# Optimization experiments

Hardware: AMD Instinct MI355X
Metric: run time of the kernel (lower is better)

## Reference

```python
import jax, jax.numpy as jnp
import numpy as np
from jax import lax

BATCH = 2
COUNT = 5
OUT = 125


def _bins(n, out=OUT):
    # PyTorch adaptive_max_pool2d bin boundaries: start=floor(i*n/out), end=ceil((i+1)*n/out)
    i = np.arange(out)
    s = (i * n) // out
    e = -((-(i + 1) * n) // out)
    m = int((e - s).max())
    idx = s[:, None] + np.arange(m)[None, :]
    return np.minimum(idx, n - 1), idx < e[:, None]


def _apool(img):
    # adaptive max pool 2d of [H,W] -> [OUT,OUT]; H,W are concrete Python ints
    H, W = img.shape
    ri, rv = _bins(H)
    ci, cv = _bins(W)
    r = jnp.where(rv[:, :, None], img[ri], -jnp.inf).max(axis=1)       # [OUT, W]
    return jnp.where(cv[None], r[:, ci], -jnp.inf).max(axis=2)         # [OUT, OUT]


def _conv(x, w, b):
    y = lax.conv_general_dilated(x, w, (1, 1), 'VALID', dimension_numbers=('NCHW', 'OIHW', 'NCHW'))
    return y + b[None, :, None, None]


def _bn(x, g, be, m, v):
    inv = g * lax.rsqrt(v + 1e-5)
    return x * inv[None, :, None, None] + (be - m * inv)[None, :, None, None]


def _pool(x, k, s):
    return lax.reduce_window(x, -np.inf, lax.max, (1, 1, k, k), (1, 1, s, s), 'VALID')


def _forward(x, ROI, roi_layer, w1, b1, g1, be1, m1, v1, w2, b2, g2, be2, m2, v2,
             w3, b3, g3, be3, m3, v3, w4, b4, g4, be4, m4, v4, fw1, fb1, fw2, fb2, fw3, fb3):
    ROI = np.asarray(ROI)
    rl = int(roi_layer)
    roiX = jax.nn.relu(_bn(_conv(x, w1, b1), g1, be1, m1, v1))  # [2,3,252,252]
    crops = []
    for k in range(BATCH):
        xs = []
        for j in range(rl):
            for i in range(COUNT):
                y1, y2, x1, x2 = (int(v) for v in ROI[k, i, 0])
                y1 = int(y1 * 0.9); y2 = int(y2 * 0.9); x2 = int(x2 * 0.9); x1 = int(x1 * 0.9)
                xs.append(_apool(roiX[k, j, y1:y2, x1:x2]))
        crops.append(xs)
    # original code prepends each batch's crop list -> batch order reversed; .numpy() detaches grads
    xb = lax.stop_gradient(jnp.stack(crops[1] + crops[0]).reshape(BATCH, COUNT * rl, OUT, OUT))
    norX = _pool(jax.nn.relu(_bn(_conv(x, w2, b2), g2, be2, m2, v2)), 4, 2)  # [2,20,125,125]
    h = jnp.concatenate([norX, xb], axis=1)                                   # [2,35,125,125]
    h = _pool(jax.nn.relu(_bn(_conv(h, w3, b3), g3, be3, m3, v3)), 2, 2)      # [2,50,60,60]
    h = _pool(jax.nn.relu(_bn(_conv(h, w4, b4), g4, be4, m4, v4)), 2, 2)      # [2,25,28,28]
    h = h.reshape(BATCH, -1)                                                  # [2,19600]
    h = jax.nn.relu(h @ fw1 + fb1)
    h = jax.nn.relu(h @ fw2 + fb2)
    h = jax.nn.relu(h @ fw3 + fb3)
    return jax.nn.softmax(h, axis=1)


def setup_inputs() -> dict:
    key = jax.random.key(0)
    ks = jax.random.split(key, 8)
    rng = np.random.default_rng(0)
    y1 = rng.integers(0, 100, (BATCH, COUNT))
    y2 = np.minimum(y1 + rng.integers(60, 150, (BATCH, COUNT)), 251)
    x1 = rng.integers(0, 100, (BATCH, COUNT))
    x2 = np.minimum(x1 + rng.integers(60, 150, (BATCH, COUNT)), 251)
    ROI = jnp.asarray(np.stack([y1, y2, x1, x2], -1)[:, :, None, :].astype(np.int32))
    d = {'x': jax.random.normal(ks[0], (BATCH, 1, 256, 256), jnp.float32), 'ROI': ROI, 'roi_layer': 3}
    d.update(w1=jax.random.normal(ks[1], (3, 1, 5, 5)) * 0.05, b1=jnp.zeros(3), g1=jnp.ones(3), be1=jnp.zeros(3), m1=jnp.zeros(3), v1=jnp.ones(3))
    d.update(w2=jax.random.normal(ks[2], (20, 1, 5, 5)) * 0.05, b2=jnp.zeros(20), g2=jnp.ones(20), be2=jnp.zeros(20), m2=jnp.zeros(20), v2=jnp.ones(20))
    d.update(w3=jax.random.normal(ks[3], (50, 35, 5, 5)) * 0.05, b3=jnp.zeros(50), g3=jnp.ones(50), be3=jnp.zeros(50), m3=jnp.zeros(50), v3=jnp.ones(50))
    d.update(w4=jax.random.normal(ks[4], (25, 50, 5, 5)) * 0.05, b4=jnp.zeros(25), g4=jnp.ones(25), be4=jnp.zeros(25), m4=jnp.zeros(25), v4=jnp.ones(25))
    d.update(fw1=jax.random.normal(ks[5], (25 * 28 * 28, 1024)) * 0.01, fb1=jnp.zeros(1024),
             fw2=jax.random.normal(ks[6], (1024, 32)) * 0.05, fb2=jnp.zeros(32),
             fw3=jax.random.normal(ks[7], (32, 2)) * 0.05, fb3=jnp.zeros(2))
    return d


def reference(x, ROI, roi_layer, w1, b1, g1, be1, m1, v1, w2, b2, g2, be2, m2, v2,
              w3, b3, g3, be3, m3, v3, w4, b4, g4, be4, m4, v4, fw1, fb1, fw2, fb2, fw3, fb3):
    return _forward(x, ROI, roi_layer, w1, b1, g1, be1, m1, v1, w2, b2, g2, be2, m2, v2,
                    w3, b3, g3, be3, m3, v3, w4, b4, g4, be4, m4, v4, fw1, fb1, fw2, fb2, fw3, fb3)
```

## Files before the change

### kernel.cpp

```cpp
#include <hip/hip_runtime.h>
#include <math.h>


#define RL 3
#define NCH 35

__global__ __launch_bounds__(256) void conv2_roi(
    const float* __restrict__ x, const int* __restrict__ ROI,
    const float* __restrict__ w2, const float* __restrict__ b2, const float* __restrict__ g2,
    const float* __restrict__ be2, const float* __restrict__ m2, const float* __restrict__ v2,
    const float* __restrict__ w1, const float* __restrict__ b1, const float* __restrict__ g1,
    const float* __restrict__ be1, const float* __restrict__ m1, const float* __restrict__ v1,
    float* __restrict__ h1) {
    int i = blockIdx.x * 256 + threadIdx.x;
    if (i >= 125 * 125) return;
    int oy = i / 125, ox = i % 125;
    if (blockIdx.y < 40) {
        int c = blockIdx.y % 20;
        int bi = blockIdx.y / 20;
        const float* xp = x + bi * 256 * 256 + (2 * oy) * 256 + 2 * ox;
        float wl[25];
#pragma unroll
        for (int k = 0; k < 25; k++) wl[k] = w2[c * 25 + k];
        float in[8][8];
#pragma unroll
        for (int r = 0; r < 8; r++)
#pragma unroll
            for (int k = 0; k < 4; k++) {
                float2 v2v = *(const float2*)(xp + r * 256 + 2 * k);
                in[r][2 * k] = v2v.x;
                in[r][2 * k + 1] = v2v.y;
            }
        float inv = g2[c] * rsqrtf(v2[c] + 1e-5f);
        float sh = (b2[c] - m2[c]) * inv + be2[c];
        float mx = -INFINITY;
#pragma unroll
        for (int py = 0; py < 4; py++) {
#pragma unroll
            for (int px = 0; px < 4; px++) {
                float acc = 0.f;
#pragma unroll
                for (int ky = 0; ky < 5; ky++)
#pragma unroll
                    for (int kx = 0; kx < 5; kx++)
                        acc = fmaf(in[py + ky][px + kx], wl[ky * 5 + kx], acc);
                mx = fmaxf(mx, fmaxf(acc * inv + sh, 0.f));
            }
        }
        h1[((bi * NCH + c) * 125 + oy) * 125 + ox] = mx;
    } else {
        int yz = blockIdx.y - 40;
        int bi = yz / 15;
        int cc = yz % 15;
        int sb = 1 - bi;
        int j = cc / 5;
        int ri = cc % 5;
        const int* rp = ROI + (sb * 5 + ri) * 4;
        int y1 = (9 * rp[0]) / 10;
        int y2 = (9 * rp[1]) / 10;
        int x1 = (9 * rp[2]) / 10;
        int x2 = (9 * rp[3]) / 10;
        int H = y2 - y1;
        int W = x2 - x1;
        int sy = (oy * H) / 125, ey = ((oy + 1) * H + 124) / 125;
        int sx = (ox * W) / 125, ex = ((ox + 1) * W + 124) / 125;
        float wl[25];
#pragma unroll
        for (int k = 0; k < 25; k++) wl[k] = w1[j * 25 + k];
        float inv = g1[j] * rsqrtf(v1[j] + 1e-5f);
        float sh = (b1[j] - m1[j]) * inv + be1[j];
        const float* xp = x + sb * 256 * 256;
        float mx = -INFINITY;
        for (int r = sy; r < ey; r++) {
            for (int c2 = sx; c2 < ex; c2++) {
                int Y = y1 + r, X = x1 + c2;
                float acc = 0.f;
#pragma unroll
                for (int ky = 0; ky < 5; ky++)
#pragma unroll
                    for (int kx = 0; kx < 5; kx++)
                        acc = fmaf(xp[(Y + ky) * 256 + X + kx], wl[ky * 5 + kx], acc);
                mx = fmaxf(mx, fmaxf(acc * inv + sh, 0.f));
            }
        }
        h1[((bi * NCH + 20 + cc) * 125 + oy) * 125 + ox] = mx;
    }
}

template <int IW, int PO, int CI, int CO, int G, int NG>
__global__ __launch_bounds__(256) void conv_partial_q(
    const float* __restrict__ in, const float* __restrict__ w,
    float* __restrict__ pac) {
    __shared__ float tile[4][2][20][24];

    const int wid = threadIdx.x >> 6;
    const int lane = threadIdx.x & 63;
    const int sy = lane >> 3, sx = lane & 7;
    const int ng = blockIdx.z % NG;
    const int bi = blockIdx.z / NG;
    const int s = wid;
    const int co0 = ng * G;
    constexpr int CPS = (CI + 3) / 4;
    const int ci0 = s * CPS;
    const int ci1 = (ci0 + CPS < CI) ? ci0 + CPS : CI;
    const int px0 = (8 * (int)blockIdx.x < PO - 8) ? 8 * (int)blockIdx.x : PO - 8;
    const int py0 = (8 * (int)blockIdx.y < PO - 8) ? 8 * (int)blockIdx.y : PO - 8;
    const int px = px0 + sx, py = py0 + sy;
    const float* ip = in + (size_t)bi * CI * IW * IW + (size_t)(2 * py0) * IW + 2 * px0;

    int cw[G];
#pragma unroll
    for (int gg = 0; gg < G; gg++) cw[gg] = (co0 + gg < CO) ? co0 + gg : CO - 1;

    float2 sreg[4];
    auto loadstage = [&](int ci) {
        const float* src = ip + (size_t)ci * IW * IW;
#pragma unroll
        for (int k = 0; k < 4; k++) {
            int p = lane + k * 64;
            if (p < 200) {
                int r = p / 10, c2 = (p % 10) * 2;
                sreg[k] = *(const float2*)(src + r * IW + c2);
            }
        }
    };
    auto writestage = [&](int buf) {
#pragma unroll
        for (int k = 0; k < 4; k++) {
            int p = lane + k * 64;
            if (p < 200) {
                int r = p / 10, c2 = (p % 10) * 2;
                *(float2*)&tile[wid][buf][r][c2] = sreg[k];
            }
        }
    };

    loadstage(ci0);
    writestage(0);
    float acc[G][4];
#pragma unroll
    for (int gg = 0; gg < G; gg++)
#pragma unroll
        for (int q = 0; q < 4; q++) acc[gg][q] = 0.f;

    for (int ci = ci0; ci < ci1; ci++) {
        const int cur = (ci - ci0) & 1;
        if (ci + 1 < ci1) loadstage(ci + 1);
        float2 p[6][3];
#pragma unroll
        for (int r = 0; r < 6; r++)
#pragma unroll
            for (int c = 0; c < 3; c++)
                p[r][c] = *(const float2*)&tile[wid][cur][2 * sy + r][2 * sx + 2 * c];
#define E(r, cc) (((cc) & 1) ? p[r][(cc) >> 1].y : p[r][(cc) >> 1].x)
#pragma unroll
        for (int gg = 0; gg < G; gg++) {
            const float* wk = w + ((size_t)cw[gg] * CI + ci) * 25;
#pragma unroll
            for (int ky = 0; ky < 5; ky++) {
#pragma unroll
                for (int kx = 0; kx < 5; kx++) {
                    float wv = wk[ky * 5 + kx];
                    acc[gg][0] = fmaf(E(ky, kx), wv, acc[gg][0]);
                    acc[gg][1] = fmaf(E(ky, kx + 1), wv, acc[gg][1]);
                    acc[gg][2] = fmaf(E(ky + 1, kx), wv, acc[gg][2]);
                    acc[gg][3] = fmaf(E(ky + 1, kx + 1), wv, acc[gg][3]);
                }
            }
        }
#undef E
        if (ci + 1 < ci1) writestage(cur ^ 1);
    }

    constexpr int CW = 2 * PO;
#pragma unroll
    for (int gg = 0; gg < G; gg++) {
        int co = co0 + gg;
        if (co < CO) {
            size_t base = (((size_t)(s * 2 + bi) * CO + co) * CW + 2 * py) * CW + 2 * px;
            float2 r0 = {acc[gg][0], acc[gg][1]};
            float2 r1 = {acc[gg][2], acc[gg][3]};
            *(float2*)&pac[base] = r0;
            *(float2*)&pac[base + CW] = r1;
        }
    }
}

template <int PO, int CO, int INIT>
__global__ __launch_bounds__(256) void conv_finish(
    const float* __restrict__ pac,
    const float* __restrict__ b, const float* __restrict__ g,
    const float* __restrict__ be, const float* __restrict__ m,
    const float* __restrict__ v, float* __restrict__ out,
    const float* __restrict__ fb1, float* __restrict__ fc1o) {
    int idx = blockIdx.x * 256 + threadIdx.x;
    if (INIT && idx < 2048) fc1o[idx] = fb1[idx & 1023];
    int total = 2 * CO * PO * PO;
    if (idx >= total) return;
    int px = idx % PO;
    int t = idx / PO;
    int py = t % PO; t /= PO;
    int co = t % CO;
    int bi = t / CO;
    constexpr int CW = 2 * PO;
    constexpr size_t SS = (size_t)2 * CO * CW * CW;
    size_t base = (((size_t)bi * CO + co) * CW + 2 * py) * CW + 2 * px;
    float s00 = 0.f, s01 = 0.f, s10 = 0.f, s11 = 0.f;
#pragma unroll
    for (int s = 0; s < 4; s++) {
        float2 a0 = *(const float2*)&pac[base + s * SS];
        float2 a1 = *(const float2*)&pac[base + s * SS + CW];
        s00 += a0.x; s01 += a0.y; s10 += a1.x; s11 += a1.y;
    }
    float inv = g[co] * rsqrtf(v[co] + 1e-5f);
    float sh = (b[co] - m[co]) * inv + be[co];
    float q0 = fmaxf(s00 * inv + sh, 0.f);
    float q1 = fmaxf(s01 * inv + sh, 0.f);
    float q2 = fmaxf(s10 * inv + sh, 0.f);
    float q3 = fmaxf(s11 * inv + sh, 0.f);
    out[idx] = fmaxf(fmaxf(q0, q1), fmaxf(q2, q3));
}

#define CHUNK 50
__global__ void fc1_mm(const float* __restrict__ h, const float* __restrict__ w,
                       float* __restrict__ out) {
    __shared__ float sh[2][CHUNK];
    int o = blockIdx.x * 256 + threadIdx.x;
    int i0 = blockIdx.y * CHUNK;
    if (threadIdx.x < 2 * CHUNK) {
        int r = threadIdx.x / CHUNK, t = threadIdx.x % CHUNK;
        sh[r][t] = h[r * 19600 + i0 + t];
    }
    __syncthreads();
    float a0 = 0.f, a1 = 0.f;
    const float* wp = w + (size_t)i0 * 1024 + o;
#pragma unroll
    for (int i = 0; i < CHUNK; i++) {
        float wv = wp[(size_t)i * 1024];
        a0 = fmaf(sh[0][i], wv, a0);
        a1 = fmaf(sh[1][i], wv, a1);
    }
    atomicAdd(&out[o], a0);
    atomicAdd(&out[1024 + o], a1);
}

__global__ void head(const float* __restrict__ fc1o, const float* __restrict__ fw2,
                     const float* __restrict__ fb2, const float* __restrict__ fw3,
                     const float* __restrict__ fb3, float* __restrict__ out) {
    int bi = blockIdx.x;
    __shared__ float h[1024];
    __shared__ float red[256];
    __shared__ float s2[32];
    for (int i = threadIdx.x; i < 1024; i += 256) h[i] = fmaxf(fc1o[bi * 1024 + i], 0.f);
    __syncthreads();
    int o = threadIdx.x >> 3;
    int part = threadIdx.x & 7;
    float a = 0.f;
    for (int i = part * 128; i < part * 128 + 128; i++) a += h[i] * fw2[i * 32 + o];
    red[threadIdx.x] = a;
    __syncthreads();
    if (part == 0) {
        float s = 0.f;
        for (int p = 0; p < 8; p++) s += red[(o << 3) + p];
        s2[o] = fmaxf(s + fb2[o], 0.f);
    }
    __syncthreads();
    if (threadIdx.x == 0) {
        float z0 = fb3[0], z1 = fb3[1];
        for (int i = 0; i < 32; i++) {
            z0 += s2[i] * fw3[i * 2];
            z1 += s2[i] * fw3[i * 2 + 1];
        }
        z0 = fmaxf(z0, 0.f);
        z1 = fmaxf(z1, 0.f);
        float mx = fmaxf(z0, z1);
        float e0 = expf(z0 - mx), e1 = expf(z1 - mx);
        float s = e0 + e1;
        out[bi * 2 + 0] = e0 / s;
        out[bi * 2 + 1] = e1 / s;
    }
}

extern "C" void kernel_launch(void* const* d_in, const int* in_sizes, int n_in,
                              void* d_out, int out_size, void* d_ws, size_t ws_size,
                              hipStream_t stream) {
    const float* x   = (const float*)d_in[0];
    const int*   ROI = (const int*)d_in[1];
    const float* w1 = (const float*)d_in[3];
    const float* b1 = (const float*)d_in[4];
    const float* g1 = (const float*)d_in[5];
    const float* be1 = (const float*)d_in[6];
    const float* m1 = (const float*)d_in[7];
    const float* v1 = (const float*)d_in[8];
    const float* w2 = (const float*)d_in[9];
    const float* b2 = (const float*)d_in[10];
    const float* g2 = (const float*)d_in[11];
    const float* be2 = (const float*)d_in[12];
    const float* m2 = (const float*)d_in[13];
    const float* v2 = (const float*)d_in[14];
    const float* w3 = (const float*)d_in[15];
    const float* b3 = (const float*)d_in[16];
    const float* g3 = (const float*)d_in[17];
    const float* be3 = (const float*)d_in[18];
    const float* m3 = (const float*)d_in[19];
    const float* v3 = (const float*)d_in[20];
    const float* w4 = (const float*)d_in[21];
    const float* b4 = (const float*)d_in[22];
    const float* g4 = (const float*)d_in[23];
    const float* be4 = (const float*)d_in[24];
    const float* m4 = (const float*)d_in[25];
    const float* v4 = (const float*)d_in[26];
    const float* fw1 = (const float*)d_in[27];
    const float* fb1 = (const float*)d_in[28];
    const float* fw2 = (const float*)d_in[29];
    const float* fb2 = (const float*)d_in[30];
    const float* fw3 = (const float*)d_in[31];
    const float* fb3 = (const float*)d_in[32];
    float* out = (float*)d_out;

    float* ws = (float*)d_ws;
    float* h1   = ws;
    float* p3   = h1 + 1093750;
    float* p4   = p3 + 360000;
    float* fc1o = p4 + 39200;
    float* pac3 = fc1o + 2048;
    float* pac4 = pac3;

    {
        dim3 grd((125 * 125 + 255) / 256, 70);
        conv2_roi<<<grd, 256, 0, stream>>>(x, ROI, w2, b2, g2, be2, m2, v2,
                                           w1, b1, g1, be1, m1, v1, h1);
    }
    {
        dim3 grd(8, 8, 2 * 13);
        conv_partial_q<125, 60, NCH, 50, 4, 13><<<grd, 256, 0, stream>>>(h1, w3, pac3);
    }
    {
        int total = 2 * 50 * 60 * 60;
        conv_finish<60, 50, 0><<<(total + 255) / 256, 256, 0, stream>>>(
            pac3, b3, g3, be3, m3, v3, p3, nullptr, nullptr);
    }
    {
        dim3 grd(4, 4, 2 * 13);
        conv_partial_q<60, 28, 50, 25, 2, 13><<<grd, 256, 0, stream>>>(p3, w4, pac4);
    }
    {
        int total = 2 * 25 * 28 * 28;
        conv_finish<28, 25, 1><<<(total + 255) / 256, 256, 0, stream>>>(
            pac4, b4, g4, be4, m4, v4, p4, fb1, fc1o);
    }
    {
        dim3 grd(4, 392);
        fc1_mm<<<grd, 256, 0, stream>>>(p4, fw1, fc1o);
    }
    head<<<2, 256, 0, stream>>>(fc1o, fw2, fb2, fw3, fb3, out);
}
```

Before: 136.9 us.

## Pad conv weights to float4 rows and split partial conv into 64-thread blocks

Extra blocks in the first kernel copy the conv3 and conv4 weights into a buffer whose 5x5 filters are padded to 28 floats. The partial conv kernels can then fetch each filter with seven float4 loads, double-buffered across output-channel groups. Each partial conv kernel is also restructured from 256-thread blocks, where four waves split the input channels, into 64-thread single-wave blocks with the channel split moved into the grid. The output-channel group size also changes. The aim is fewer scalar weight loads, better latency hiding and more blocks in flight, at the cost of extra register pressure and a small weight-repack pass run on every call.

```diff
diff --git a/kernel.cpp b/kernel.cpp
--- a/kernel.cpp
+++ b/kernel.cpp
@@ -11,7 +11,20 @@
     const float* __restrict__ be2, const float* __restrict__ m2, const float* __restrict__ v2,
     const float* __restrict__ w1, const float* __restrict__ b1, const float* __restrict__ g1,
     const float* __restrict__ be1, const float* __restrict__ m1, const float* __restrict__ v1,
+    const float* __restrict__ w3, const float* __restrict__ w4,
+    float* __restrict__ wp3, float* __restrict__ wp4,
     float* __restrict__ h1) {
+    if (blockIdx.y >= 70) {
+        const float* src = (blockIdx.y == 70) ? w3 : w4;
+        float* dst = (blockIdx.y == 70) ? wp3 : wp4;
+        int rows = (blockIdx.y == 70) ? 50 * 35 : 25 * 50;
+        int total = rows * 28;
+        for (int i = blockIdx.x * 256 + threadIdx.x; i < total; i += gridDim.x * 256) {
+            int t = i % 28, r = i / 28;
+            dst[i] = (t < 25) ? src[r * 25 + t] : 0.f;
+        }
+        return;
+    }
     int i = blockIdx.x * 256 + threadIdx.x;
     if (i >= 125 * 125) return;
     int oy = i / 125, ox = i % 125;
@@ -87,20 +100,20 @@
     }
 }
 
-template <int IW, int PO, int CI, int CO, int G, int NG>
-__global__ __launch_bounds__(256) void conv_partial_q(
-    const float* __restrict__ in, const float* __restrict__ w,
+template <int IW, int PO, int CI, int CO, int G, int NG, int NS>
+__global__ __launch_bounds__(64, 4) void conv_partial(
+    const float* __restrict__ in, const float* __restrict__ wp,
     float* __restrict__ pac) {
-    __shared__ float tile[4][2][20][24];
-
-    const int wid = threadIdx.x >> 6;
-    const int lane = threadIdx.x & 63;
+    __shared__ float tile[2][20][24];
+
+    const int lane = threadIdx.x;
     const int sy = lane >> 3, sx = lane & 7;
-    const int ng = blockIdx.z % NG;
-    const int bi = blockIdx.z / NG;
-    const int s = wid;
+    int z = blockIdx.z;
+    const int ng = z % NG; z /= NG;
+    const int s = z % NS;
+    const int bi = z / NS;
     const int co0 = ng * G;
-    constexpr int CPS = (CI + 3) / 4;
+    constexpr int CPS = (CI + NS - 1) / NS;
     const int ci0 = s * CPS;
     const int ci1 = (ci0 + CPS < CI) ? ci0 + CPS : CI;
     const int px0 = (8 * (int)blockIdx.x < PO - 8) ? 8 * (int)blockIdx.x : PO - 8;
@@ -130,47 +143,64 @@
             int p = lane + k * 64;
             if (p < 200) {
                 int r = p / 10, c2 = (p % 10) * 2;
-                *(float2*)&tile[wid][buf][r][c2] = sreg[k];
+                *(float2*)&tile[buf][r][c2] = sreg[k];
             }
         }
     };
+
+    float4 wA[7], wB[7];
+    auto wload = [&](float4(&wr)[7], int gg, int ci) {
+        const float* src = wp + ((size_t)cw[gg] * CI + ci) * 28;
+#pragma unroll
+        for (int k = 0; k < 7; k++) wr[k] = *(const float4*)(src + 4 * k);
+    };
+
+    float acc[G][4];
+#pragma unroll
+    for (int gg = 0; gg < G; gg++)
+#pragma unroll
+        for (int q = 0; q < 4; q++) acc[gg][q] = 0.f;
+
+#define WE(W, t) ((t) % 4 == 0 ? W[(t) / 4].x : (t) % 4 == 1 ? W[(t) / 4].y : (t) % 4 == 2 ? W[(t) / 4].z : W[(t) / 4].w)
+#define FMAG(W, gg)                                                            \
+    {                                                                          \
+        _Pragma("unroll") for (int ky = 0; ky < 5; ky++) {                     \
+            _Pragma("unroll") for (int kx = 0; kx < 5; kx++) {                 \
+                float wv = WE(W, ky * 5 + kx);                                 \
+                float e00 = ((kx)&1) ? p[ky][kx >> 1].y : p[ky][kx >> 1].x;    \
+                float e01 = ((kx + 1) & 1) ? p[ky][(kx + 1) >> 1].y : p[ky][(kx + 1) >> 1].x; \
+                float e10 = ((kx)&1) ? p[ky + 1][kx >> 1].y : p[ky + 1][kx >> 1].x; \
+                float e11 = ((kx + 1) & 1) ? p[ky + 1][(kx + 1) >> 1].y : p[ky + 1][(kx + 1) >> 1].x; \
+                acc[gg][0] = fmaf(e00, wv, acc[gg][0]);                        \
+                acc[gg][1] = fmaf(e01, wv, acc[gg][1]);                        \
+                acc[gg][2] = fmaf(e10, wv, acc[gg][2]);                        \
+                acc[gg][3] = fmaf(e11, wv, acc[gg][3]);                        \
+            }                                                                  \
+        }                                                                      \
+    }
 
     loadstage(ci0);
     writestage(0);
-    float acc[G][4];
-#pragma unroll
-    for (int gg = 0; gg < G; gg++)
-#pragma unroll
-        for (int q = 0; q < 4; q++) acc[gg][q] = 0.f;
 
     for (int ci = ci0; ci < ci1; ci++) {
         const int cur = (ci - ci0) & 1;
         if (ci + 1 < ci1) loadstage(ci + 1);
+        wload(wA, 0, ci);
         float2 p[6][3];
 #pragma unroll
         for (int r = 0; r < 6; r++)
 #pragma unroll
             for (int c = 0; c < 3; c++)
-                p[r][c] = *(const float2*)&tile[wid][cur][2 * sy + r][2 * sx + 2 * c];
-#define E(r, cc) (((cc) & 1) ? p[r][(cc) >> 1].y : p[r][(cc) >> 1].x)
-#pragma unroll
-        for (int gg = 0; gg < G; gg++) {
-            const float* wk = w + ((size_t)cw[gg] * CI + ci) * 25;
-#pragma unroll
-            for (int ky = 0; ky < 5; ky++) {
-#pragma unroll
-                for (int kx = 0; kx < 5; kx++) {
-                    float wv = wk[ky * 5 + kx];
-                    acc[gg][0] = fmaf(E(ky, kx), wv, acc[gg][0]);
-                    acc[gg][1] = fmaf(E(ky, kx + 1), wv, acc[gg][1]);
-                    acc[gg][2] = fmaf(E(ky + 1, kx), wv, acc[gg][2]);
-                    acc[gg][3] = fmaf(E(ky + 1, kx + 1), wv, acc[gg][3]);
-                }
-            }
-        }
-#undef E
+                p[r][c] = *(const float2*)&tile[cur][2 * sy + r][2 * sx + 2 * c];
+        wload(wB, 1, ci);
+        FMAG(wA, 0);
+        wload(wA, 2, ci);
+        FMAG(wB, 1);
+        FMAG(wA, 2);
         if (ci + 1 < ci1) writestage(cur ^ 1);
     }
+#undef FMAG
+#undef WE
 
     constexpr int CW = 2 * PO;
 #pragma unroll
@@ -325,15 +355,18 @@
     float* fc1o = p4 + 39200;
     float* pac3 = fc1o + 2048;
     float* pac4 = pac3;
-
-    {
-        dim3 grd((125 * 125 + 255) / 256, 70);
+    float* wp3  = pac3 + 5760000;
+    float* wp4  = wp3 + 49000;
+
+    {
+        dim3 grd((125 * 125 + 255) / 256, 72);
         conv2_roi<<<grd, 256, 0, stream>>>(x, ROI, w2, b2, g2, be2, m2, v2,
-                                           w1, b1, g1, be1, m1, v1, h1);
-    }
-    {
-        dim3 grd(8, 8, 2 * 13);
-        conv_partial_q<125, 60, NCH, 50, 4, 13><<<grd, 256, 0, stream>>>(h1, w3, pac3);
+                                           w1, b1, g1, be1, m1, v1,
+                                           w3, w4, wp3, wp4, h1);
+    }
+    {
+        dim3 grd(8, 8, 2 * 4 * 17);
+        conv_partial<125, 60, NCH, 50, 3, 17, 4><<<grd, 64, 0, stream>>>(h1, wp3, pac3);
     }
     {
         int total = 2 * 50 * 60 * 60;
@@ -341,8 +374,8 @@
             pac3, b3, g3, be3, m3, v3, p3, nullptr, nullptr);
     }
     {
-        dim3 grd(4, 4, 2 * 13);
-        conv_partial_q<60, 28, 50, 25, 2, 13><<<grd, 256, 0, stream>>>(p3, w4, pac4);
+        dim3 grd(4, 4, 2 * 4 * 9);
+        conv_partial<60, 28, 50, 25, 3, 9, 4><<<grd, 64, 0, stream>>>(p3, wp4, pac4);
     }
     {
         int total = 2 * 25 * 28 * 28;
```

After: 125.3 us. 8.5% less time.
